# Kernel tuning notes

Hardware: AMD Instinct MI355X
Metric: run time of the kernel (lower is better)

The kernel has to match this reference:

```python
import jax, jax.numpy as jnp
import numpy as np

B, L, C, H = 8, 1024, 512, 8
D = C // H  # head_size = 64


def setup_inputs() -> dict:
    key = jax.random.key(0)
    k1, k2, k3, k4, k5, k6 = jax.random.split(key, 6)
    x = jax.random.normal(k1, (B, L, C), dtype=jnp.float32)
    adj = jax.random.randint(k2, (B, L, L), 0, 2).astype(jnp.float32)
    distance = jax.random.randint(k3, (B, L, L), 0, 3).astype(jnp.float32)
    # nn.Linear(dim, 3*dim, bias=False): stored as y = x @ W; init ~ U(-1/sqrt(C), 1/sqrt(C))
    bound = 1.0 / np.sqrt(C)
    w_qkv = jax.random.uniform(k4, (C, 3 * C), minval=-bound, maxval=bound, dtype=jnp.float32)
    w_proj = jax.random.uniform(k5, (C, C), minval=-bound, maxval=bound, dtype=jnp.float32)
    # struct_gamma is zero-init in the module; use small random values so biases are exercised
    gamma = 0.1 * jax.random.normal(k6, (H, 5), dtype=jnp.float32)
    return {"x": x, "adj": adj, "distance": distance,
            "w_qkv": w_qkv, "w_proj": w_proj, "gamma": gamma}


def reference(x, adj, distance, w_qkv, w_proj, gamma):
    b, l, c = x.shape
    scale = jnp.asarray(np.sqrt(D), x.dtype)
    qkv = x @ w_qkv                                    # [B,L,3C]
    q, k, v = jnp.split(qkv, 3, axis=-1)
    q = q.reshape(b, l, H, D).transpose(0, 2, 1, 3)     # [B,H,L,D]
    k = k.reshape(b, l, H, D).transpose(0, 2, 1, 3)
    v = v.reshape(b, l, H, D).transpose(0, 2, 1, 3)
    s = jnp.einsum('bhid,bhjd->bhij', q, k) / scale     # [B,H,L,L]

    # has_cls=True: zero row 0 and col 0 of adj
    adj_local = adj.at[:, 0, :].set(0.0).at[:, :, 0].set(0.0)
    adj_t = adj_local.transpose(0, 2, 1)
    b_fwd = adj_local                                   # direct edges
    b_bwd = adj_t
    b_dist_fwd = (distance > 0).astype(x.dtype)         # multi-hop reachability
    b_dist_bwd = (distance.transpose(0, 2, 1) > 0).astype(x.dtype)
    b_struct = (jnp.einsum('bik,bjk->bij', adj_local, adj_local) > 0).astype(x.dtype)

    biases = jnp.stack([b_fwd, b_bwd, b_dist_fwd, b_dist_bwd, b_struct], axis=1)  # [B,5,L,L]
    s = s + jnp.einsum('hk,bkij->bhij', gamma, biases)

    attn = jax.nn.softmax(s, axis=-1)
    out = jnp.einsum('bhij,bhjd->bhid', attn, v)        # [B,H,L,D]
    out = out.transpose(0, 2, 1, 3).reshape(b, l, c)
    return out @ w_proj
```

## Files before the change

kernel.cpp:

```cpp
#include <hip/hip_runtime.h>
#include <hip/hip_bf16.h>
#include <stdint.h>

#define NB 8
#define NL 1024
#define NC 512
#define NH 8
#define ND 64

typedef __attribute__((ext_vector_type(8))) short short8;
typedef __attribute__((ext_vector_type(4))) float f32x4;
typedef unsigned long long u64;

__device__ __forceinline__ short f2bf(float f) {
  union { float f; uint32_t u; } v; v.f = f;
  uint32_t r = v.u + 0x7FFFu + ((v.u >> 16) & 1u);
  return (short)(r >> 16);
}

#if __has_builtin(__builtin_amdgcn_exp2f)
#define EXP2(x) __builtin_amdgcn_exp2f(x)
#else
#define EXP2(x) exp2f(x)
#endif

#define MFMA16(a, b, c) __builtin_amdgcn_mfma_f32_16x16x32_bf16((a), (b), (c), 0, 0, 0)

__global__ __launch_bounds__(256) void pack_k(const float* __restrict__ adj,
                                              const float* __restrict__ dist,
                                              u64* __restrict__ padj,
                                              u64* __restrict__ pdist) {
  int row = blockIdx.x;
  int i = row & (NL - 1);
  int wv = threadIdx.x >> 6, lane = threadIdx.x & 63;
  const float* asrc = adj + (size_t)row * NL;
  const float* dsrc = dist + (size_t)row * NL;
  #pragma unroll
  for (int it = 0; it < 4; it++) {
    int j = wv * 256 + it * 64 + lane;
    float a = asrc[j];
    float d = dsrc[j];
    u64 am = __ballot((a != 0.0f) && (i != 0) && (j != 0));
    u64 dm = __ballot(d > 0.0f);
    if (lane == 0) {
      padj[(size_t)row * 16 + wv * 4 + it] = am;
      pdist[(size_t)row * 16 + wv * 4 + it] = dm;
    }
  }
}

__global__ __launch_bounds__(256) void bits_k(const u64* __restrict__ padj,
                                              const u64* __restrict__ pdist,
                                              unsigned char* __restrict__ bits) {
  __shared__ u64 Pi[64][17], Pj[64][17];
  __shared__ u64 DiW[64], DjW[64];
  int b = blockIdx.z, i0 = blockIdx.y * 64, j0 = blockIdx.x * 64;
  int t = threadIdx.x;
  int jw = j0 >> 6, iw = i0 >> 6;
  const u64* pa = padj + (size_t)b * NL * 16;
  const u64* pd = pdist + (size_t)b * NL * 16;
  #pragma unroll
  for (int s = 0; s < 4; s++) {
    int idx = s * 256 + t; int r = idx >> 4, w = idx & 15;
    Pi[r][w] = pa[(size_t)(i0 + r) * 16 + w];
    Pj[r][w] = pa[(size_t)(j0 + r) * 16 + w];
  }
  if (t < 64) DiW[t] = pd[(size_t)(i0 + t) * 16 + jw];
  else if (t < 128) DjW[t - 64] = pd[(size_t)(j0 + t - 64) * 16 + iw];
  __syncthreads();
  const size_t base = (size_t)b * NL * NL;
  int jj0 = (t & 15) * 4;
  #pragma unroll
  for (int s = 0; s < 4; s++) {
    int ii = (t >> 4) + s * 16;
    u64 fwdw = Pi[ii][jw];
    u64 dfw = DiW[ii];
    uint32_t acc = 0;
    #pragma unroll
    for (int q = 0; q < 4; q++) {
      int jj = jj0 + q;
      unsigned v = 0;
      v |= (unsigned)((fwdw >> jj) & 1);
      v |= (unsigned)((Pj[jj][iw] >> ii) & 1) << 1;
      v |= (unsigned)((dfw >> jj) & 1) << 2;
      v |= (unsigned)((DjW[jj] >> ii) & 1) << 3;
      #pragma unroll 1
      for (int w = 0; w < 16; w++) {
        if (Pi[ii][w] & Pj[jj][w]) { v |= 16; break; }
      }
      acc |= v << (8 * q);
    }
    *(uint32_t*)&bits[base + (size_t)(i0 + ii) * NL + j0 + jj0] = acc;
  }
}

__global__ __launch_bounds__(256) void wcvt_k(const float* __restrict__ w,
                                              unsigned short* __restrict__ wt,
                                              int Ndim) {
  __shared__ short T[64][68];
  int k0 = blockIdx.y * 64, n0 = blockIdx.x * 64;
  int t = threadIdx.x;
  {
    int r = t >> 2, c0 = (t & 3) * 16;
    const float* src = w + (size_t)(k0 + r) * Ndim + n0 + c0;
    float4 a0 = *(const float4*)src;
    float4 a1 = *(const float4*)(src + 4);
    float4 a2 = *(const float4*)(src + 8);
    float4 a3 = *(const float4*)(src + 12);
    short8 s0, s1;
    s0[0] = f2bf(a0.x); s0[1] = f2bf(a0.y); s0[2] = f2bf(a0.z); s0[3] = f2bf(a0.w);
    s0[4] = f2bf(a1.x); s0[5] = f2bf(a1.y); s0[6] = f2bf(a1.z); s0[7] = f2bf(a1.w);
    s1[0] = f2bf(a2.x); s1[1] = f2bf(a2.y); s1[2] = f2bf(a2.z); s1[3] = f2bf(a2.w);
    s1[4] = f2bf(a3.x); s1[5] = f2bf(a3.y); s1[6] = f2bf(a3.z); s1[7] = f2bf(a3.w);
    *(short8*)&T[r][c0]     = s0;
    *(short8*)&T[r][c0 + 8] = s1;
  }
  __syncthreads();
  #pragma unroll
  for (int it = 0; it < 2; it++) {
    int nn = (t >> 3) + it * 32, kc = (t & 7) * 8;
    short8 v;
    #pragma unroll
    for (int j = 0; j < 8; j++) v[j] = T[kc + j][nn];
    *(short8*)(wt + (size_t)(n0 + nn) * NC + k0 + kc) = v;
  }
}

__global__ __launch_bounds__(256) void qkv_gemm_k(const float* __restrict__ x,
                                                  const unsigned short* __restrict__ wqT,
                                                  unsigned short* __restrict__ qb,
                                                  unsigned short* __restrict__ kb,
                                                  unsigned short* __restrict__ vb) {
  __shared__ short Al[64][40];
  __shared__ short Bl[64][40];
  int t = threadIdx.x;
  int wv = t >> 6, lane = t & 63, lg = lane >> 4, lm = lane & 15;
  int wr = wv >> 1, wc = wv & 1;
  int M0 = blockIdx.y * 64, N0 = blockIdx.x * 64;
  f32x4 zero4 = {0.f, 0.f, 0.f, 0.f};
  f32x4 acc[2][2] = {{zero4, zero4}, {zero4, zero4}};
  for (int k0 = 0; k0 < NC; k0 += 32) {
    {
      int row = t >> 2, cc = (t & 3) * 8;
      const float* src = x + (size_t)(M0 + row) * NC + k0 + cc;
      float4 v0 = *(const float4*)src;
      float4 v1 = *(const float4*)(src + 4);
      short8 s8;
      s8[0] = f2bf(v0.x); s8[1] = f2bf(v0.y); s8[2] = f2bf(v0.z); s8[3] = f2bf(v0.w);
      s8[4] = f2bf(v1.x); s8[5] = f2bf(v1.y); s8[6] = f2bf(v1.z); s8[7] = f2bf(v1.w);
      *(short8*)&Al[row][cc] = s8;
    }
    {
      int n = t >> 2, kk = (t & 3) * 8;
      *(short8*)&Bl[n][kk] =
          *(const short8*)(wqT + (size_t)(N0 + n) * NC + k0 + kk);
    }
    __syncthreads();
    short8 af[2], bfr[2];
    af[0] = *(short8*)&Al[wr * 32 + lm][lg * 8];
    af[1] = *(short8*)&Al[wr * 32 + 16 + lm][lg * 8];
    bfr[0] = *(short8*)&Bl[wc * 32 + lm][lg * 8];
    bfr[1] = *(short8*)&Bl[wc * 32 + 16 + lm][lg * 8];
    #pragma unroll
    for (int mi = 0; mi < 2; mi++)
      #pragma unroll
      for (int ni = 0; ni < 2; ni++)
        acc[mi][ni] = MFMA16(af[mi], bfr[ni], acc[mi][ni]);
    __syncthreads();
  }
  #pragma unroll
  for (int mi = 0; mi < 2; mi++)
    #pragma unroll
    for (int ni = 0; ni < 2; ni++)
      #pragma unroll
      for (int r = 0; r < 4; r++) {
        int m = M0 + wr * 32 + mi * 16 + lg * 4 + r;
        int n = N0 + wc * 32 + ni * 16 + lm;
        int which = n >> 9, c = n & 511;
        int h = c >> 6, d = c & 63;
        int bb = m >> 10, ll = m & 1023;
        float val = acc[mi][ni][r];
        unsigned short* dst;
        if (which == 0) { dst = qb; val *= 0.125f; }
        else dst = (which == 1) ? kb : vb;
        dst[(((size_t)bb * NH + h) * NL + ll) * ND + d] = (unsigned short)f2bf(val);
      }
}

__global__ __launch_bounds__(256) void vt_k(const unsigned short* __restrict__ vb,
                                            unsigned short* __restrict__ vtb) {
  __shared__ short T[64][68];
  int b = blockIdx.z, h = blockIdx.y, l0 = blockIdx.x * 64;
  int t = threadIdx.x;
  const size_t bh = (size_t)b * NH + h;
  {
    int r = t >> 2, c0 = (t & 3) * 16;
    const unsigned short* src = vb + ((bh * NL) + l0 + r) * ND + c0;
    *(short8*)&T[r][c0]     = *(const short8*)src;
    *(short8*)&T[r][c0 + 8] = *(const short8*)(src + 8);
  }
  __syncthreads();
  #pragma unroll
  for (int it = 0; it < 2; it++) {
    int d = (t >> 3) + it * 32, lc = (t & 7) * 8;
    short8 v;
    #pragma unroll
    for (int j = 0; j < 8; j++) v[j] = T[lc + j][d];
    *(short8*)(vtb + (bh * ND + d) * NL + l0 + lc) = v;
  }
}

__global__ __launch_bounds__(256) void attn_k(const unsigned short* __restrict__ qb,
                                              const unsigned short* __restrict__ kb,
                                              const unsigned short* __restrict__ vtb,
                                              const unsigned char* __restrict__ bits,
                                              const float* __restrict__ gamma,
                                              unsigned short* __restrict__ ao) {
  __shared__ short Kl[64][72];
  __shared__ short Vt[64][72];
  __shared__ short Pl[64][68];
  __shared__ float lut[32];
  int b = blockIdx.z, h = blockIdx.y, q0 = blockIdx.x * 64;
  int t = threadIdx.x, wv = t >> 6, lane = t & 63, lg = lane >> 4, lm = lane & 15;
  const float LOG2E = 1.4426950408889634f;
  if (t < 32) {
    float s = 0.f;
    #pragma unroll
    for (int k = 0; k < 5; k++) if ((t >> k) & 1) s += gamma[h * 5 + k];
    lut[t] = s * LOG2E - 8.0f;
  }
  const size_t bh = ((size_t)b * NH + h) * NL;
  const size_t bhD = ((size_t)b * NH + h) * ND;
  short8 qf[2];
  {
    const unsigned short* src = qb + (bh + q0 + wv * 16 + lm) * ND + lg * 8;
    qf[0] = *(const short8*)src;
    qf[1] = *(const short8*)(src + 32);
  }
  f32x4 zero4 = {0.f, 0.f, 0.f, 0.f};
  f32x4 oacc[4] = {zero4, zero4, zero4, zero4};
  float lsum[4] = {0.f, 0.f, 0.f, 0.f};
  __syncthreads();
  for (int j0 = 0; j0 < NL; j0 += 64) {
    {
      int r = t >> 2, cc = (t & 3) * 16;
      const unsigned short* ks = kb + (bh + j0 + r) * ND + cc;
      *(short8*)&Kl[r][cc]     = *(const short8*)ks;
      *(short8*)&Kl[r][cc + 8] = *(const short8*)(ks + 8);
      const unsigned short* vs = vtb + (bhD + r) * NL + j0 + cc;
      *(short8*)&Vt[r][cc]     = *(const short8*)vs;
      *(short8*)&Vt[r][cc + 8] = *(const short8*)(vs + 8);
    }
    __syncthreads();
    f32x4 sf[4];
    #pragma unroll
    for (int ni = 0; ni < 4; ni++) {
      short8 b0 = *(short8*)&Kl[ni * 16 + lm][lg * 8];
      short8 b1 = *(short8*)&Kl[ni * 16 + lm][32 + lg * 8];
      f32x4 c = {0.f, 0.f, 0.f, 0.f};
      c = MFMA16(qf[0], b0, c);
      c = MFMA16(qf[1], b1, c);
      sf[ni] = c;
    }
    #pragma unroll
    for (int ni = 0; ni < 4; ni++)
      #pragma unroll
      for (int r = 0; r < 4; r++) {
        int qi = q0 + wv * 16 + lg * 4 + r;
        int kj = j0 + ni * 16 + lm;
        unsigned char bt = bits[((size_t)b * NL + qi) * NL + kj];
        float p = EXP2(fmaf(sf[ni][r], LOG2E, lut[bt & 31]));
        lsum[r] += p;
        Pl[wv * 16 + lg * 4 + r][ni * 16 + lm] = f2bf(p);
      }
    short8 pa0 = *(short8*)&Pl[wv * 16 + lm][lg * 8];
    short8 pa1 = *(short8*)&Pl[wv * 16 + lm][32 + lg * 8];
    #pragma unroll
    for (int di = 0; di < 4; di++) {
      short8 vb0 = *(short8*)&Vt[di * 16 + lm][lg * 8];
      short8 vb1 = *(short8*)&Vt[di * 16 + lm][32 + lg * 8];
      oacc[di] = MFMA16(pa0, vb0, oacc[di]);
      oacc[di] = MFMA16(pa1, vb1, oacc[di]);
    }
    __syncthreads();
  }
  float inv[4];
  #pragma unroll
  for (int r = 0; r < 4; r++) {
    float s = lsum[r];
    s += __shfl_xor(s, 1);
    s += __shfl_xor(s, 2);
    s += __shfl_xor(s, 4);
    s += __shfl_xor(s, 8);
    inv[r] = 1.0f / s;
  }
  #pragma unroll
  for (int di = 0; di < 4; di++)
    #pragma unroll
    for (int r = 0; r < 4; r++) {
      int qi = q0 + wv * 16 + lg * 4 + r;
      int d = di * 16 + lm;
      ao[((size_t)b * NL + qi) * NC + h * ND + d] =
          (unsigned short)f2bf(oacc[di][r] * inv[r]);
    }
}

__global__ __launch_bounds__(256) void proj_gemm_k(const unsigned short* __restrict__ ao,
                                                   const unsigned short* __restrict__ wpT,
                                                   float* __restrict__ out) {
  __shared__ short Al[64][40];
  __shared__ short Bl[64][40];
  int t = threadIdx.x;
  int wv = t >> 6, lane = t & 63, lg = lane >> 4, lm = lane & 15;
  int wr = wv >> 1, wc = wv & 1;
  int M0 = blockIdx.y * 64, N0 = blockIdx.x * 64;
  f32x4 zero4 = {0.f, 0.f, 0.f, 0.f};
  f32x4 acc[2][2] = {{zero4, zero4}, {zero4, zero4}};
  for (int k0 = 0; k0 < NC; k0 += 32) {
    {
      int row = t >> 2, cc = (t & 3) * 8;
      *(short8*)&Al[row][cc] = *(const short8*)(ao + (size_t)(M0 + row) * NC + k0 + cc);
    }
    {
      int n = t >> 2, kk = (t & 3) * 8;
      *(short8*)&Bl[n][kk] =
          *(const short8*)(wpT + (size_t)(N0 + n) * NC + k0 + kk);
    }
    __syncthreads();
    short8 af[2], bfr[2];
    af[0] = *(short8*)&Al[wr * 32 + lm][lg * 8];
    af[1] = *(short8*)&Al[wr * 32 + 16 + lm][lg * 8];
    bfr[0] = *(short8*)&Bl[wc * 32 + lm][lg * 8];
    bfr[1] = *(short8*)&Bl[wc * 32 + 16 + lm][lg * 8];
    #pragma unroll
    for (int mi = 0; mi < 2; mi++)
      #pragma unroll
      for (int ni = 0; ni < 2; ni++)
        acc[mi][ni] = MFMA16(af[mi], bfr[ni], acc[mi][ni]);
    __syncthreads();
  }
  #pragma unroll
  for (int mi = 0; mi < 2; mi++)
    #pragma unroll
    for (int ni = 0; ni < 2; ni++)
      #pragma unroll
      for (int r = 0; r < 4; r++) {
        int m = M0 + wr * 32 + mi * 16 + lg * 4 + r;
        int n = N0 + wc * 32 + ni * 16 + lm;
        out[(size_t)m * NC + n] = acc[mi][ni][r];
      }
}

extern "C" void kernel_launch(void* const* d_in, const int* in_sizes, int n_in,
                              void* d_out, int out_size, void* d_ws, size_t ws_size,
                              hipStream_t stream) {
  (void)in_sizes; (void)n_in; (void)out_size; (void)ws_size;
  const float* x      = (const float*)d_in[0];
  const float* adj    = (const float*)d_in[1];
  const float* dist   = (const float*)d_in[2];
  const float* w_qkv  = (const float*)d_in[3];
  const float* w_proj = (const float*)d_in[4];
  const float* gamma  = (const float*)d_in[5];
  float* out = (float*)d_out;

  char* ws = (char*)d_ws;
  size_t off = 0;
  auto take = [&](size_t bytes) -> char* {
    char* p = ws + off;
    off += (bytes + 255) & ~(size_t)255;
    return p;
  };
  unsigned short* qb = (unsigned short*)take((size_t)NB * NH * NL * ND * 2);
  unsigned short* kb = (unsigned short*)take((size_t)NB * NH * NL * ND * 2);
  unsigned short* vb = (unsigned short*)take((size_t)NB * NH * NL * ND * 2);
  unsigned short* vtb = (unsigned short*)take((size_t)NB * NH * NL * ND * 2);
  u64* padj  = (u64*)take((size_t)NB * NL * 16 * 8);
  u64* pdist = (u64*)take((size_t)NB * NL * 16 * 8);
  unsigned char* bits = (unsigned char*)take((size_t)NB * NL * NL);
  unsigned short* ao = (unsigned short*)take((size_t)NB * NL * NC * 2);
  unsigned short* wqT = (unsigned short*)take((size_t)3 * NC * NC * 2);
  unsigned short* wpT = (unsigned short*)take((size_t)NC * NC * 2);

  pack_k<<<dim3(NB * NL), dim3(256), 0, stream>>>(adj, dist, padj, pdist);
  wcvt_k<<<dim3(24, 8), dim3(256), 0, stream>>>(w_qkv, wqT, 3 * NC);
  wcvt_k<<<dim3(8, 8), dim3(256), 0, stream>>>(w_proj, wpT, NC);
  qkv_gemm_k<<<dim3(24, 128), dim3(256), 0, stream>>>(x, wqT, qb, kb, vb);
  vt_k<<<dim3(16, NH, NB), dim3(256), 0, stream>>>(vb, vtb);
  bits_k<<<dim3(16, 16, NB), dim3(256), 0, stream>>>(padj, pdist, bits);
  attn_k<<<dim3(16, NH, NB), dim3(256), 0, stream>>>(qb, kb, vtb, bits, gamma, ao);
  proj_gemm_k<<<dim3(8, 128), dim3(256), 0, stream>>>(ao, wpT, out);
}
```

Measured before the change: 268.0 us.

## Double-buffer K/V tiles with register prefetch and compute bias in registers

The attention loop now prefetches the next K/V tile into registers before computing on the current one, then stores it into a second LDS buffer. This drops to one barrier per iteration and overlaps global loads with the MFMA work. The bias lookup table in LDS is replaced by per-head gamma scalars held in registers and summed with conditional selects. The bias bytes for a tile are also loaded up front into registers. In exchange, LDS use doubles for K/V, register pressure rises, and there is more ALU work per score element.

```diff
diff --git a/kernel.cpp b/kernel.cpp
--- a/kernel.cpp
+++ b/kernel.cpp
@@ -216,19 +216,17 @@
                                               const unsigned char* __restrict__ bits,
                                               const float* __restrict__ gamma,
                                               unsigned short* __restrict__ ao) {
-  __shared__ short Kl[64][72];
-  __shared__ short Vt[64][72];
+  __shared__ short Kl[2][64][72];
+  __shared__ short Vt[2][64][72];
   __shared__ short Pl[64][68];
-  __shared__ float lut[32];
   int b = blockIdx.z, h = blockIdx.y, q0 = blockIdx.x * 64;
   int t = threadIdx.x, wv = t >> 6, lane = t & 63, lg = lane >> 4, lm = lane & 15;
   const float LOG2E = 1.4426950408889634f;
-  if (t < 32) {
-    float s = 0.f;
-    #pragma unroll
-    for (int k = 0; k < 5; k++) if ((t >> k) & 1) s += gamma[h * 5 + k];
-    lut[t] = s * LOG2E - 8.0f;
-  }
+  float G0 = gamma[h * 5 + 0] * LOG2E;
+  float G1 = gamma[h * 5 + 1] * LOG2E;
+  float G2 = gamma[h * 5 + 2] * LOG2E;
+  float G3 = gamma[h * 5 + 3] * LOG2E;
+  float G4 = gamma[h * 5 + 4] * LOG2E;
   const size_t bh = ((size_t)b * NH + h) * NL;
   const size_t bhD = ((size_t)b * NH + h) * ND;
   short8 qf[2];
@@ -237,26 +235,40 @@
     qf[0] = *(const short8*)src;
     qf[1] = *(const short8*)(src + 32);
   }
+  int sr = t >> 2, scc = (t & 3) * 16;
+  const unsigned short* krow = kb + (bh + sr) * ND + scc;
+  const unsigned short* vrow = vtb + (bhD + sr) * NL + scc;
+  const unsigned char* brow = bits + ((size_t)b * NL + q0 + wv * 16 + lg * 4) * NL + lm;
+  short8 kr0 = *(const short8*)(krow);
+  short8 kr1 = *(const short8*)(krow + 8);
+  short8 vr0 = *(const short8*)(vrow);
+  short8 vr1 = *(const short8*)(vrow + 8);
+  *(short8*)&Kl[0][sr][scc] = kr0;  *(short8*)&Kl[0][sr][scc + 8] = kr1;
+  *(short8*)&Vt[0][sr][scc] = vr0;  *(short8*)&Vt[0][sr][scc + 8] = vr1;
+  __syncthreads();
   f32x4 zero4 = {0.f, 0.f, 0.f, 0.f};
   f32x4 oacc[4] = {zero4, zero4, zero4, zero4};
   float lsum[4] = {0.f, 0.f, 0.f, 0.f};
-  __syncthreads();
-  for (int j0 = 0; j0 < NL; j0 += 64) {
-    {
-      int r = t >> 2, cc = (t & 3) * 16;
-      const unsigned short* ks = kb + (bh + j0 + r) * ND + cc;
-      *(short8*)&Kl[r][cc]     = *(const short8*)ks;
-      *(short8*)&Kl[r][cc + 8] = *(const short8*)(ks + 8);
-      const unsigned short* vs = vtb + (bhD + r) * NL + j0 + cc;
-      *(short8*)&Vt[r][cc]     = *(const short8*)vs;
-      *(short8*)&Vt[r][cc + 8] = *(const short8*)(vs + 8);
-    }
-    __syncthreads();
+  for (int ti = 0; ti < 16; ti++) {
+    int cur = ti & 1;
+    int j0 = ti * 64;
+    if (ti < 15) {
+      kr0 = *(const short8*)(krow + (size_t)(j0 + 64) * ND);
+      kr1 = *(const short8*)(krow + (size_t)(j0 + 64) * ND + 8);
+      vr0 = *(const short8*)(vrow + j0 + 64);
+      vr1 = *(const short8*)(vrow + j0 + 64 + 8);
+    }
+    unsigned bq[16];
+    #pragma unroll
+    for (int ni = 0; ni < 4; ni++)
+      #pragma unroll
+      for (int r = 0; r < 4; r++)
+        bq[ni * 4 + r] = brow[(size_t)r * NL + j0 + ni * 16];
     f32x4 sf[4];
     #pragma unroll
     for (int ni = 0; ni < 4; ni++) {
-      short8 b0 = *(short8*)&Kl[ni * 16 + lm][lg * 8];
-      short8 b1 = *(short8*)&Kl[ni * 16 + lm][32 + lg * 8];
+      short8 b0 = *(short8*)&Kl[cur][ni * 16 + lm][lg * 8];
+      short8 b1 = *(short8*)&Kl[cur][ni * 16 + lm][32 + lg * 8];
       f32x4 c = {0.f, 0.f, 0.f, 0.f};
       c = MFMA16(qf[0], b0, c);
       c = MFMA16(qf[1], b1, c);
@@ -266,10 +278,14 @@
     for (int ni = 0; ni < 4; ni++)
       #pragma unroll
       for (int r = 0; r < 4; r++) {
-        int qi = q0 + wv * 16 + lg * 4 + r;
-        int kj = j0 + ni * 16 + lm;
-        unsigned char bt = bits[((size_t)b * NL + qi) * NL + kj];
-        float p = EXP2(fmaf(sf[ni][r], LOG2E, lut[bt & 31]));
+        unsigned bt = bq[ni * 4 + r];
+        float bias = -8.0f;
+        bias += (bt & 1u) ? G0 : 0.0f;
+        bias += (bt & 2u) ? G1 : 0.0f;
+        bias += (bt & 4u) ? G2 : 0.0f;
+        bias += (bt & 8u) ? G3 : 0.0f;
+        bias += (bt & 16u) ? G4 : 0.0f;
+        float p = EXP2(fmaf(sf[ni][r], LOG2E, bias));
         lsum[r] += p;
         Pl[wv * 16 + lg * 4 + r][ni * 16 + lm] = f2bf(p);
       }
@@ -277,12 +293,18 @@
     short8 pa1 = *(short8*)&Pl[wv * 16 + lm][32 + lg * 8];
     #pragma unroll
     for (int di = 0; di < 4; di++) {
-      short8 vb0 = *(short8*)&Vt[di * 16 + lm][lg * 8];
-      short8 vb1 = *(short8*)&Vt[di * 16 + lm][32 + lg * 8];
+      short8 vb0 = *(short8*)&Vt[cur][di * 16 + lm][lg * 8];
+      short8 vb1 = *(short8*)&Vt[cur][di * 16 + lm][32 + lg * 8];
       oacc[di] = MFMA16(pa0, vb0, oacc[di]);
       oacc[di] = MFMA16(pa1, vb1, oacc[di]);
     }
-    __syncthreads();
+    if (ti < 15) {
+      *(short8*)&Kl[cur ^ 1][sr][scc] = kr0;
+      *(short8*)&Kl[cur ^ 1][sr][scc + 8] = kr1;
+      *(short8*)&Vt[cur ^ 1][sr][scc] = vr0;
+      *(short8*)&Vt[cur ^ 1][sr][scc + 8] = vr1;
+      __syncthreads();
+    }
   }
   float inv[4];
   #pragma unroll
```

Result: slower. 288.0 us (+7.5%).
